# Performance work log

Measured on AMD Instinct MI355X. Metric: run time of the kernel, lower is better.

The kernel has to match this reference:

```python
import jax, jax.numpy as jnp
import numpy as np

D_MODEL = 1024
N_HEADS = 16
HEAD_DIM = D_MODEL // N_HEADS


def setup_inputs() -> dict:
    key = jax.random.key(0)
    kx, kq, kk, kv, ko = jax.random.split(key, 5)
    B, T = 4, 2048
    s = 1.0 / np.sqrt(D_MODEL)
    return {
        "x": jax.random.normal(kx, (B, T, D_MODEL), dtype=jnp.float32),
        "W_Q": jax.random.normal(kq, (D_MODEL, D_MODEL), dtype=jnp.float32) * s,
        "W_K": jax.random.normal(kk, (D_MODEL, D_MODEL), dtype=jnp.float32) * s,
        "W_V": jax.random.normal(kv, (D_MODEL, D_MODEL), dtype=jnp.float32) * s,
        "W_O": jax.random.normal(ko, (D_MODEL, D_MODEL), dtype=jnp.float32) * s,
    }


def reference(x, W_Q, W_K, W_V, W_O):
    B, T, C = x.shape
    H, hd = N_HEADS, HEAD_DIM
    # nn.Linear applies x @ W.T; W_* here are the [out,in] weight matrices.
    def proj(W):
        return (x @ W.T).reshape(B, T, H, hd).transpose(0, 2, 1, 3)  # [B,H,T,hd]
    q, k, v = proj(W_Q), proj(W_K), proj(W_V)
    scale = 1.0 / np.sqrt(hd).astype(np.float32)
    attn = jnp.einsum("bhqd,bhkd->bhqk", q, k) * scale  # [B,H,T,T]
    causal = jnp.tril(jnp.ones((T, T), dtype=bool))
    attn = jnp.where(causal, attn, -jnp.inf)
    attn = jax.nn.softmax(attn, axis=-1)
    out = jnp.einsum("bhqk,bhkd->bhqd", attn, v)  # [B,H,T,hd]
    out = out.transpose(0, 2, 1, 3).reshape(B, T, C)
    return out @ W_O.T
```

## Files before the change

kernel.cpp:

```cpp
#include <hip/hip_runtime.h>
#include <hip/hip_bf16.h>
#include <stdint.h>


typedef __attribute__((ext_vector_type(8))) short short8;
typedef __attribute__((ext_vector_type(4))) short short4v;
typedef __attribute__((ext_vector_type(4))) float floatx4;

#define LOG2E 1.4426950408889634f

__device__ __forceinline__ void gload_lds16(const void* g, void* l) {
  __builtin_amdgcn_global_load_lds(
      (const __attribute__((address_space(1))) void*)g,
      (__attribute__((address_space(3))) void*)l, 16, 0, 0);
}

__device__ __forceinline__ short f2bf(float f) {
  __hip_bfloat16 h = __float2bfloat16(f);
  return *reinterpret_cast<short*>(&h);
}

__global__ __launch_bounds__(256) void cvt_f32_bf16(const float* __restrict__ src,
                                                    short* __restrict__ dst, int n4,
                                                    float scale) {
  const int i = blockIdx.x * blockDim.x + threadIdx.x;
  if (i >= n4) return;
  const float4 v = reinterpret_cast<const float4*>(src)[i];
  short4v o;
  o.x = f2bf(v.x * scale); o.y = f2bf(v.y * scale);
  o.z = f2bf(v.z * scale); o.w = f2bf(v.w * scale);
  reinterpret_cast<short4v*>(dst)[i] = o;
}

__global__ __launch_bounds__(256) void cvt_weights(const float* __restrict__ wq,
                                                   const float* __restrict__ wk,
                                                   const float* __restrict__ wv,
                                                   const float* __restrict__ wo,
                                                   short* __restrict__ dst0,
                                                   float qscale) {
  const int y = blockIdx.y;
  const float* src = (y == 0) ? wq : (y == 1) ? wk : (y == 2) ? wv : wo;
  const float scale = (y == 0) ? qscale : 1.0f;
  short* dst = dst0 + (size_t)y * 1048576;
  const int i = blockIdx.x * blockDim.x + threadIdx.x;
  const float4 v = reinterpret_cast<const float4*>(src)[i];
  short4v o;
  o.x = f2bf(v.x * scale); o.y = f2bf(v.y * scale);
  o.z = f2bf(v.z * scale); o.w = f2bf(v.w * scale);
  reinterpret_cast<short4v*>(&dst[i * 4])[0] = o;
}

template <int MODE>
__device__ __forceinline__ void gemm256_body(const short* __restrict__ A,
                                             const short* __restrict__ B,
                                             void* __restrict__ Cout,
                                             int m0, int n0,
                                             short* __restrict__ la0,
                                             short* __restrict__ la1,
                                             short* __restrict__ la2,
                                             short* __restrict__ lb0,
                                             short* __restrict__ lb1,
                                             short* __restrict__ lb2) {
  const int tid = threadIdx.x;
  const int lane = tid & 63;
  const int w = tid >> 6;
  const int wm = w >> 1, wn = w & 1;
  const int lrow = lane & 15, lgrp = lane >> 4;

  floatx4 acc[4][4] = {};

  const int srow = tid >> 3;
  const int scb = (tid & 7) ^ (srow & 7);
  const short* ag = A + (size_t)(m0 + srow) * 1024 + scb * 8;
  const short* bg = B + (size_t)(n0 + srow) * 1024 + scb * 8;

  auto stage6 = [&](short* la, short* lb) {
    gload_lds16(ag, la + tid * 8);
    gload_lds16(ag + 64 * 1024, la + (512 + tid) * 8);
    gload_lds16(ag + 128 * 1024, la + (1024 + tid) * 8);
    gload_lds16(ag + 192 * 1024, la + (1536 + tid) * 8);
    gload_lds16(bg, lb + tid * 8);
    gload_lds16(bg + 64 * 1024, lb + (512 + tid) * 8);
    ag += 64; bg += 64;
  };

  short8 af[2][4];
  auto loadA = [&](const short* la) {
#pragma unroll
    for (int mf = 0; mf < 4; ++mf) {
      const int row = wm * 64 + mf * 16 + lrow;
#pragma unroll
      for (int kk = 0; kk < 2; ++kk)
        af[kk][mf] = *reinterpret_cast<const short8*>(
            &la[row * 64 + (((kk * 4 + lgrp) ^ (row & 7)) * 8)]);
    }
  };
  auto half = [&](const short* lb, int nh) {
    short8 bf[2][2];
#pragma unroll
    for (int nf = 0; nf < 2; ++nf) {
      const int row = wn * 64 + (nh * 2 + nf) * 16 + lrow;
#pragma unroll
      for (int kk = 0; kk < 2; ++kk)
        bf[kk][nf] = *reinterpret_cast<const short8*>(
            &lb[row * 64 + (((kk * 4 + lgrp) ^ (row & 7)) * 8)]);
    }
    __builtin_amdgcn_s_setprio(1);
#pragma unroll
    for (int kk = 0; kk < 2; ++kk)
#pragma unroll
      for (int mf = 0; mf < 4; ++mf)
#pragma unroll
        for (int nf = 0; nf < 2; ++nf)
          acc[mf][nh * 2 + nf] = __builtin_amdgcn_mfma_f32_16x16x32_bf16(
              af[kk][mf], bf[kk][nf], acc[mf][nh * 2 + nf], 0, 0, 0);
    __builtin_amdgcn_s_setprio(0);
  };
  auto compute = [&](const short* la, const short* lb) {
    loadA(la);
    half(lb, 0);
    half(lb, 1);
  };
  auto iter_main = [&](const short* ca, const short* cb, short* na, short* nb) {
    __builtin_amdgcn_sched_barrier(0);
    asm volatile("s_waitcnt vmcnt(6)" ::: "memory");
    __builtin_amdgcn_s_barrier();
    __builtin_amdgcn_sched_barrier(0);
    stage6(na, nb);
    compute(ca, cb);
  };

  stage6(la0, lb0);
  stage6(la1, lb1);

#pragma unroll 1
  for (int kt = 0; kt < 12; kt += 3) {
    iter_main(la0, lb0, la2, lb2);
    iter_main(la1, lb1, la0, lb0);
    iter_main(la2, lb2, la1, lb1);
  }
  iter_main(la0, lb0, la2, lb2);
  iter_main(la1, lb1, la0, lb0);
  {
    __builtin_amdgcn_sched_barrier(0);
    asm volatile("s_waitcnt vmcnt(6)" ::: "memory");
    __builtin_amdgcn_s_barrier();
    __builtin_amdgcn_sched_barrier(0);
    compute(la2, lb2);
  }
  {
    __builtin_amdgcn_sched_barrier(0);
    asm volatile("s_waitcnt vmcnt(0)" ::: "memory");
    __builtin_amdgcn_s_barrier();
    __builtin_amdgcn_sched_barrier(0);
    compute(la0, lb0);
  }

#pragma unroll
  for (int mf = 0; mf < 4; ++mf) {
#pragma unroll
    for (int nf = 0; nf < 4; ++nf) {
      if (MODE == 2) {
        short4v pk;
#pragma unroll
        for (int r = 0; r < 4; ++r) pk[r] = f2bf(acc[mf][nf][r]);
        const int t0 = m0 + wm * 64 + mf * 16 + lgrp * 4;
        const int ch = n0 + wn * 64 + nf * 16 + lrow;
        const int bh = ((t0 >> 11) << 4) + (ch >> 6);
        short* Vt = reinterpret_cast<short*>(Cout);
        *reinterpret_cast<short4v*>(
            &Vt[(size_t)bh * 131072 + (size_t)(ch & 63) * 2048 + (t0 & 2047)]) = pk;
      } else {
#pragma unroll
        for (int r = 0; r < 4; ++r) {
          const int grow = m0 + wm * 64 + mf * 16 + lgrp * 4 + r;
          const int gcol = n0 + wn * 64 + nf * 16 + lrow;
          if (MODE == 1)
            reinterpret_cast<short*>(Cout)[(size_t)grow * 1024 + gcol] = f2bf(acc[mf][nf][r]);
          else
            reinterpret_cast<float*>(Cout)[(size_t)grow * 1024 + gcol] = acc[mf][nf][r];
        }
      }
    }
  }
}

__global__ __launch_bounds__(512) void gemm_qkv(
    const short* __restrict__ xb, const short* __restrict__ wq, const short* __restrict__ wk,
    const short* __restrict__ wv, short* __restrict__ Qb, short* __restrict__ Kb,
    short* __restrict__ Vt) {
  __shared__ short lds_a[3][256 * 64];
  __shared__ short lds_b[3][128 * 64];
  const int flat = blockIdx.x;
  const int xcd = flat & 7, rest = flat >> 3;
  const int nblk = rest & 7, pg = rest >> 3;
  const int panel = pg * 8 + xcd;
  const int m = panel & 31, z = panel >> 5;
  const int m0 = m * 256, n0 = nblk * 128;
  if (z == 0)
    gemm256_body<1>(xb, wq, Qb, m0, n0, lds_a[0], lds_a[1], lds_a[2],
                    lds_b[0], lds_b[1], lds_b[2]);
  else if (z == 1)
    gemm256_body<1>(xb, wk, Kb, m0, n0, lds_a[0], lds_a[1], lds_a[2],
                    lds_b[0], lds_b[1], lds_b[2]);
  else
    gemm256_body<2>(xb, wv, Vt, m0, n0, lds_a[0], lds_a[1], lds_a[2],
                    lds_b[0], lds_b[1], lds_b[2]);
}

__global__ __launch_bounds__(512) void gemm_out(const short* __restrict__ Ob,
                                                const short* __restrict__ wo,
                                                float* __restrict__ out) {
  __shared__ short lds_a[3][256 * 64];
  __shared__ short lds_b[3][128 * 64];
  const int flat = blockIdx.x;
  const int xcd = flat & 7, rest = flat >> 3;
  const int nblk = rest & 7, pg = rest >> 3;
  const int panel = pg * 8 + xcd;
  gemm256_body<0>(Ob, wo, out, panel * 256, nblk * 128,
                  lds_a[0], lds_a[1], lds_a[2], lds_b[0], lds_b[1], lds_b[2]);
}

__global__ __launch_bounds__(256, 4) void attn_fwd(const short* __restrict__ Q,
                                                   const short* __restrict__ K,
                                                   const short* __restrict__ Vt,
                                                   short* __restrict__ O) {
  __shared__ short lds_k[2][64 * 64];
  __shared__ short lds_v[2][64 * 64];
  __shared__ short lds_p[4][16 * 64];

  const int tid = threadIdx.x;
  const int lane = tid & 63;
  const int w = tid >> 6;
  const int lrow = lane & 15, lgrp = lane >> 4;
  const int flat = blockIdx.x;
  const int bh = flat & 63;
  const int p = flat >> 6;
  const int b = bh >> 4, h = bh & 15;

  const size_t base = (size_t)b * 2048 * 1024 + h * 64;
  const size_t vbase = (size_t)bh * 131072;

  const int srow = tid >> 3;
  const int scb = (tid & 7) ^ (srow & 7);
  const size_t koff = (size_t)srow * 1024 + scb * 8;
  const size_t voff = (size_t)srow * 2048 + scb * 8;
  short* const kd0 = &lds_k[0][tid * 8];
  short* const kd1 = &lds_k[1][tid * 8];
  short* const vd0 = &lds_v[0][tid * 8];
  short* const vd1 = &lds_v[1][tid * 8];

  auto stageK = [&](short* ldst, const short* gsrc) {
    gload_lds16(gsrc, ldst);
    gload_lds16(gsrc + 32 * 1024, ldst + 2048);
  };
  auto stageV = [&](short* ldst, const short* gsrc) {
    gload_lds16(gsrc, ldst);
    gload_lds16(gsrc + 32 * 2048, ldst + 2048);
  };

#pragma unroll 1
  for (int pass = 0; pass < 2; ++pass) {
    const int qc = pass == 0 ? (31 - p) : p;
    const int qw = qc * 64 + w * 16;
    const int nkb = qc + 1;

    short8 qf0, qf1;
    {
      const short* qp = Q + base + (size_t)(qw + lrow) * 1024 + lgrp * 8;
      qf0 = *reinterpret_cast<const short8*>(qp);
      qf1 = *reinterpret_cast<const short8*>(qp + 32);
    }

    floatx4 oacc[4] = {};
    float lsum = 0.f;

    const short* kg = K + base + koff;
    const short* vg = Vt + vbase + voff;

    auto body = [&](int kb, const short* __restrict__ ldsk,
                    const short* __restrict__ ldsv) {
      floatx4 s[4];
      __builtin_amdgcn_s_setprio(1);
#pragma unroll
      for (int nf = 0; nf < 4; ++nf) {
        const short8 kf0 = *reinterpret_cast<const short8*>(
            &ldsk[(nf * 16 + lrow) * 64 + ((lgrp) ^ (lrow & 7)) * 8]);
        const short8 kf1 = *reinterpret_cast<const short8*>(
            &ldsk[(nf * 16 + lrow) * 64 + ((4 + lgrp) ^ (lrow & 7)) * 8]);
        floatx4 z = {};
        z = __builtin_amdgcn_mfma_f32_16x16x32_bf16(kf0, qf0, z, 0, 0, 0);
        z = __builtin_amdgcn_mfma_f32_16x16x32_bf16(kf1, qf1, z, 0, 0, 0);
        s[nf] = z;
      }
      __builtin_amdgcn_s_setprio(0);

      if (kb == qc) {
#pragma unroll
        for (int nf = 0; nf < 4; ++nf)
#pragma unroll
          for (int r = 0; r < 4; ++r)
            if (nf * 16 + lgrp * 4 + r > w * 16 + lrow) s[nf][r] = -1e30f;
      }

#pragma unroll
      for (int nf = 0; nf < 4; ++nf) {
        const float p0 = __builtin_amdgcn_exp2f(s[nf][0]);
        const float p1 = __builtin_amdgcn_exp2f(s[nf][1]);
        const float p2 = __builtin_amdgcn_exp2f(s[nf][2]);
        const float p3 = __builtin_amdgcn_exp2f(s[nf][3]);
        lsum += (p0 + p1) + (p2 + p3);
        short4v pk;
        pk.x = f2bf(p0); pk.y = f2bf(p1); pk.z = f2bf(p2); pk.w = f2bf(p3);
        const int c8 = (nf * 4 + lgrp) ^ ((lrow & 7) << 1);
        *reinterpret_cast<short4v*>(&lds_p[w][lrow * 64 + c8 * 4]) = pk;
      }

      short8 pa0, pa1;
      {
        const int c0 = (lgrp) ^ (lrow & 7);
        const int c1 = (4 + lgrp) ^ (lrow & 7);
        pa0 = *reinterpret_cast<const short8*>(&lds_p[w][lrow * 64 + c0 * 8]);
        pa1 = *reinterpret_cast<const short8*>(&lds_p[w][lrow * 64 + c1 * 8]);
      }
      __builtin_amdgcn_s_setprio(1);
#pragma unroll
      for (int nf = 0; nf < 4; ++nf) {
        const short8 vf0 = *reinterpret_cast<const short8*>(
            &ldsv[(nf * 16 + lrow) * 64 + ((lgrp) ^ (lrow & 7)) * 8]);
        const short8 vf1 = *reinterpret_cast<const short8*>(
            &ldsv[(nf * 16 + lrow) * 64 + ((4 + lgrp) ^ (lrow & 7)) * 8]);
        oacc[nf] = __builtin_amdgcn_mfma_f32_16x16x32_bf16(pa0, vf0, oacc[nf], 0, 0, 0);
        oacc[nf] = __builtin_amdgcn_mfma_f32_16x16x32_bf16(pa1, vf1, oacc[nf], 0, 0, 0);
      }
      __builtin_amdgcn_s_setprio(0);
    };

    stageK(kd0, kg); kg += 65536;
    stageV(vd0, vg); vg += 64;
    __syncthreads();

#pragma unroll 1
    for (int kb = 0; kb < nkb; kb += 2) {
      if (kb + 1 < nkb) { stageK(kd1, kg); kg += 65536; stageV(vd1, vg); vg += 64; }
      body(kb, lds_k[0], lds_v[0]);
      __syncthreads();
      if (kb + 1 >= nkb) break;
      if (kb + 2 < nkb) { stageK(kd0, kg); kg += 65536; stageV(vd0, vg); vg += 64; }
      body(kb + 1, lds_k[1], lds_v[1]);
      __syncthreads();
    }

    lsum += __shfl_xor(lsum, 16, 64);
    lsum += __shfl_xor(lsum, 32, 64);
#pragma unroll
    for (int r = 0; r < 4; ++r) {
      const float linv = 1.0f / __shfl(lsum, lgrp * 4 + r, 64);
      const int t = qw + lgrp * 4 + r;
#pragma unroll
      for (int nf = 0; nf < 4; ++nf)
        O[base + (size_t)t * 1024 + nf * 16 + lrow] = f2bf(oacc[nf][r] * linv);
    }
  }
}

extern "C" void kernel_launch(void* const* d_in, const int* in_sizes, int n_in,
                              void* d_out, int out_size, void* d_ws, size_t ws_size,
                              hipStream_t stream) {
  const float* x  = (const float*)d_in[0];
  const float* Wq = (const float*)d_in[1];
  const float* Wk = (const float*)d_in[2];
  const float* Wv = (const float*)d_in[3];
  const float* Wo = (const float*)d_in[4];

  uint8_t* ws = (uint8_t*)d_ws;
  short* xb  = (short*)(ws + 0);
  short* wqb = (short*)(ws + 16777216);
  short* wkb = (short*)(ws + 18874368);
  short* wvb = (short*)(ws + 20971520);
  short* wob = (short*)(ws + 23068672);
  short* Qb  = (short*)(ws + 25165824);
  short* Kb  = (short*)(ws + 41943040);
  short* Vt  = (short*)(ws + 58720256);
  short* Ob  = (short*)(ws + 75497472);
  if (ws_size < 92274688ull) return;

  const float qscale = 0.125f * LOG2E;

  cvt_f32_bf16<<<8192, 256, 0, stream>>>(x, xb, 2097152, 1.0f);
  cvt_weights<<<dim3(1024, 4), 256, 0, stream>>>(Wq, Wk, Wv, Wo, wqb, qscale);

  gemm_qkv<<<768, 512, 0, stream>>>(xb, wqb, wkb, wvb, Qb, Kb, Vt);
  attn_fwd<<<1024, 256, 0, stream>>>(Qb, Kb, Vt, Ob);
  gemm_out<<<256, 512, 0, stream>>>(Ob, wob, (float*)d_out);
}
```

Baseline: 159.2 us.

## Interleave LDS reads, prefetch issues and MFMA quadrants with wave barriers in GEMM

Restructures the GEMM main loop. Each K-tile is now split into four MFMA quadrants, with LDS fragment reads and the global-to-LDS prefetch loads interleaved between them. Extra s_barrier calls keep the waves in lockstep, in a ping-pong style schedule. The aim is to overlap LDS traffic and global load issue with matrix-core work and to reduce register pressure by holding fewer fragments live. The cost is more barriers per tile, which can stall waves. The swizzle expression was also changed from row&7 to lrow&7.

```diff
diff --git a/kernel.cpp b/kernel.cpp
--- a/kernel.cpp
+++ b/kernel.cpp
@@ -84,50 +84,103 @@
     ag += 64; bg += 64;
   };
 
-  short8 af[2][4];
-  auto loadA = [&](const short* la) {
-#pragma unroll
-    for (int mf = 0; mf < 4; ++mf) {
-      const int row = wm * 64 + mf * 16 + lrow;
-#pragma unroll
-      for (int kk = 0; kk < 2; ++kk)
-        af[kk][mf] = *reinterpret_cast<const short8*>(
-            &la[row * 64 + (((kk * 4 + lgrp) ^ (row & 7)) * 8)]);
-    }
-  };
-  auto half = [&](const short* lb, int nh) {
-    short8 bf[2][2];
-#pragma unroll
-    for (int nf = 0; nf < 2; ++nf) {
-      const int row = wn * 64 + (nh * 2 + nf) * 16 + lrow;
-#pragma unroll
-      for (int kk = 0; kk < 2; ++kk)
-        bf[kk][nf] = *reinterpret_cast<const short8*>(
-            &lb[row * 64 + (((kk * 4 + lgrp) ^ (row & 7)) * 8)]);
-    }
+  auto rdA = [&](const short* la, int mf, int kk) {
+    const int row = wm * 64 + mf * 16 + lrow;
+    return *reinterpret_cast<const short8*>(
+        &la[row * 64 + (((kk * 4 + lgrp) ^ (lrow & 7)) * 8)]);
+  };
+  auto rdB = [&](const short* lb, int nf, int kk) {
+    const int row = wn * 64 + nf * 16 + lrow;
+    return *reinterpret_cast<const short8*>(
+        &lb[row * 64 + (((kk * 4 + lgrp) ^ (lrow & 7)) * 8)]);
+  };
+
+  auto tile = [&](const short* la, const short* lb, short* na, short* nb, bool pf) {
+    short8 a0[2][2], a1[2][2], b0[2][2], b1[2][2];
+#pragma unroll
+    for (int kk = 0; kk < 2; ++kk) {
+      a0[kk][0] = rdA(la, 0, kk); a0[kk][1] = rdA(la, 1, kk);
+      b0[kk][0] = rdB(lb, 0, kk); b0[kk][1] = rdB(lb, 1, kk);
+    }
+    if (pf) {
+      gload_lds16(ag, na + tid * 8);
+      gload_lds16(ag + 64 * 1024, na + (512 + tid) * 8);
+    }
+    __builtin_amdgcn_sched_barrier(0);
+    __builtin_amdgcn_s_barrier();
     __builtin_amdgcn_s_setprio(1);
 #pragma unroll
     for (int kk = 0; kk < 2; ++kk)
 #pragma unroll
-      for (int mf = 0; mf < 4; ++mf)
-#pragma unroll
-        for (int nf = 0; nf < 2; ++nf)
-          acc[mf][nh * 2 + nf] = __builtin_amdgcn_mfma_f32_16x16x32_bf16(
-              af[kk][mf], bf[kk][nf], acc[mf][nh * 2 + nf], 0, 0, 0);
+      for (int i = 0; i < 2; ++i)
+#pragma unroll
+        for (int j = 0; j < 2; ++j)
+          acc[i][j] = __builtin_amdgcn_mfma_f32_16x16x32_bf16(a0[kk][i], b0[kk][j], acc[i][j], 0, 0, 0);
     __builtin_amdgcn_s_setprio(0);
-  };
-  auto compute = [&](const short* la, const short* lb) {
-    loadA(la);
-    half(lb, 0);
-    half(lb, 1);
-  };
-  auto iter_main = [&](const short* ca, const short* cb, short* na, short* nb) {
-    __builtin_amdgcn_sched_barrier(0);
-    asm volatile("s_waitcnt vmcnt(6)" ::: "memory");
-    __builtin_amdgcn_s_barrier();
-    __builtin_amdgcn_sched_barrier(0);
-    stage6(na, nb);
-    compute(ca, cb);
+    __builtin_amdgcn_sched_barrier(0);
+    __builtin_amdgcn_s_barrier();
+#pragma unroll
+    for (int kk = 0; kk < 2; ++kk) {
+      b1[kk][0] = rdB(lb, 2, kk); b1[kk][1] = rdB(lb, 3, kk);
+    }
+    if (pf) {
+      gload_lds16(ag + 128 * 1024, na + (1024 + tid) * 8);
+      gload_lds16(ag + 192 * 1024, na + (1536 + tid) * 8);
+    }
+    __builtin_amdgcn_sched_barrier(0);
+    __builtin_amdgcn_s_barrier();
+    __builtin_amdgcn_s_setprio(1);
+#pragma unroll
+    for (int kk = 0; kk < 2; ++kk)
+#pragma unroll
+      for (int i = 0; i < 2; ++i)
+#pragma unroll
+        for (int j = 0; j < 2; ++j)
+          acc[i][2 + j] = __builtin_amdgcn_mfma_f32_16x16x32_bf16(a0[kk][i], b1[kk][j], acc[i][2 + j], 0, 0, 0);
+    __builtin_amdgcn_s_setprio(0);
+    __builtin_amdgcn_sched_barrier(0);
+    __builtin_amdgcn_s_barrier();
+#pragma unroll
+    for (int kk = 0; kk < 2; ++kk) {
+      a1[kk][0] = rdA(la, 2, kk); a1[kk][1] = rdA(la, 3, kk);
+    }
+    if (pf) {
+      gload_lds16(bg, nb + tid * 8);
+      gload_lds16(bg + 64 * 1024, nb + (512 + tid) * 8);
+      ag += 64; bg += 64;
+    }
+    __builtin_amdgcn_sched_barrier(0);
+    __builtin_amdgcn_s_barrier();
+    __builtin_amdgcn_s_setprio(1);
+#pragma unroll
+    for (int kk = 0; kk < 2; ++kk)
+#pragma unroll
+      for (int i = 0; i < 2; ++i)
+#pragma unroll
+        for (int j = 0; j < 2; ++j)
+          acc[2 + i][j] = __builtin_amdgcn_mfma_f32_16x16x32_bf16(a1[kk][i], b0[kk][j], acc[2 + i][j], 0, 0, 0);
+    __builtin_amdgcn_s_setprio(0);
+    __builtin_amdgcn_sched_barrier(0);
+    __builtin_amdgcn_s_barrier();
+    __builtin_amdgcn_s_setprio(1);
+#pragma unroll
+    for (int kk = 0; kk < 2; ++kk)
+#pragma unroll
+      for (int i = 0; i < 2; ++i)
+#pragma unroll
+        for (int j = 0; j < 2; ++j)
+          acc[2 + i][2 + j] = __builtin_amdgcn_mfma_f32_16x16x32_bf16(a1[kk][i], b1[kk][j], acc[2 + i][2 + j], 0, 0, 0);
+    __builtin_amdgcn_s_setprio(0);
+  };
+
+  auto tiletop = [&](int n) {
+    __builtin_amdgcn_sched_barrier(0);
+    if (n == 0)
+      asm volatile("s_waitcnt vmcnt(0)" ::: "memory");
+    else
+      asm volatile("s_waitcnt vmcnt(6)" ::: "memory");
+    __builtin_amdgcn_s_barrier();
+    __builtin_amdgcn_sched_barrier(0);
   };
 
   stage6(la0, lb0);
@@ -135,26 +188,14 @@
 
 #pragma unroll 1
   for (int kt = 0; kt < 12; kt += 3) {
-    iter_main(la0, lb0, la2, lb2);
-    iter_main(la1, lb1, la0, lb0);
-    iter_main(la2, lb2, la1, lb1);
+    tiletop(6); tile(la0, lb0, la2, lb2, true);
+    tiletop(6); tile(la1, lb1, la0, lb0, true);
+    tiletop(6); tile(la2, lb2, la1, lb1, true);
   }
-  iter_main(la0, lb0, la2, lb2);
-  iter_main(la1, lb1, la0, lb0);
-  {
-    __builtin_amdgcn_sched_barrier(0);
-    asm volatile("s_waitcnt vmcnt(6)" ::: "memory");
-    __builtin_amdgcn_s_barrier();
-    __builtin_amdgcn_sched_barrier(0);
-    compute(la2, lb2);
-  }
-  {
-    __builtin_amdgcn_sched_barrier(0);
-    asm volatile("s_waitcnt vmcnt(0)" ::: "memory");
-    __builtin_amdgcn_s_barrier();
-    __builtin_amdgcn_sched_barrier(0);
-    compute(la0, lb0);
-  }
+  tiletop(6); tile(la0, lb0, la2, lb2, true);
+  tiletop(6); tile(la1, lb1, la0, lb0, true);
+  tiletop(6); tile(la2, lb2, nullptr, nullptr, false);
+  tiletop(0); tile(la0, lb0, nullptr, nullptr, false);
 
 #pragma unroll
   for (int mf = 0; mf < 4; ++mf) {
```

Result: slower. 163.8 us (+2.9%).

## Halve GEMM K-tile to 32 with new LDS swizzle and deeper iteration count

Applied to the files above, without the earlier changes.

The shared GEMM body now stages K-tiles of 32 instead of 64 bf16 elements, which halves the LDS footprint per buffer and uses a 4-column XOR swizzle. Each tile issues 3 async global-to-LDS loads instead of 6 and runs 16 MFMAs per barrier, over 32 iterations instead of 16. The smaller LDS footprint could allow more blocks per CU. In exchange it doubles the number of barriers and waitcnt synchronisations per K sweep and shortens the prefetch distance in bytes.

```diff
diff --git a/kernel.cpp b/kernel.cpp
--- a/kernel.cpp
+++ b/kernel.cpp
@@ -69,92 +69,63 @@
 
   floatx4 acc[4][4] = {};
 
-  const int srow = tid >> 3;
-  const int scb = (tid & 7) ^ (srow & 7);
+  const int srow = tid >> 2;
+  const int scb = (tid & 3) ^ (srow & 3) ^ ((srow & 4) >> 1);
   const short* ag = A + (size_t)(m0 + srow) * 1024 + scb * 8;
   const short* bg = B + (size_t)(n0 + srow) * 1024 + scb * 8;
 
-  auto stage6 = [&](short* la, short* lb) {
+  auto stage3 = [&](short* la, short* lb) {
     gload_lds16(ag, la + tid * 8);
-    gload_lds16(ag + 64 * 1024, la + (512 + tid) * 8);
-    gload_lds16(ag + 128 * 1024, la + (1024 + tid) * 8);
-    gload_lds16(ag + 192 * 1024, la + (1536 + tid) * 8);
+    gload_lds16(ag + 128 * 1024, la + (512 + tid) * 8);
     gload_lds16(bg, lb + tid * 8);
-    gload_lds16(bg + 64 * 1024, lb + (512 + tid) * 8);
-    ag += 64; bg += 64;
-  };
-
-  short8 af[2][4];
-  auto loadA = [&](const short* la) {
+    ag += 32; bg += 32;
+  };
+
+  const int slA = (lgrp ^ (lrow & 3) ^ ((lrow & 4) >> 1)) * 8;
+
+  auto tile = [&](const short* la, const short* lb, short* na, short* nb, bool pf) {
+    if (pf) stage3(na, nb);
+    short8 af[4], bf[4];
 #pragma unroll
     for (int mf = 0; mf < 4; ++mf) {
       const int row = wm * 64 + mf * 16 + lrow;
-#pragma unroll
-      for (int kk = 0; kk < 2; ++kk)
-        af[kk][mf] = *reinterpret_cast<const short8*>(
-            &la[row * 64 + (((kk * 4 + lgrp) ^ (row & 7)) * 8)]);
-    }
-  };
-  auto half = [&](const short* lb, int nh) {
-    short8 bf[2][2];
-#pragma unroll
-    for (int nf = 0; nf < 2; ++nf) {
-      const int row = wn * 64 + (nh * 2 + nf) * 16 + lrow;
-#pragma unroll
-      for (int kk = 0; kk < 2; ++kk)
-        bf[kk][nf] = *reinterpret_cast<const short8*>(
-            &lb[row * 64 + (((kk * 4 + lgrp) ^ (row & 7)) * 8)]);
+      af[mf] = *reinterpret_cast<const short8*>(&la[row * 32 + slA]);
+    }
+#pragma unroll
+    for (int nf = 0; nf < 4; ++nf) {
+      const int row = wn * 64 + nf * 16 + lrow;
+      bf[nf] = *reinterpret_cast<const short8*>(&lb[row * 32 + slA]);
     }
     __builtin_amdgcn_s_setprio(1);
 #pragma unroll
-    for (int kk = 0; kk < 2; ++kk)
-#pragma unroll
-      for (int mf = 0; mf < 4; ++mf)
-#pragma unroll
-        for (int nf = 0; nf < 2; ++nf)
-          acc[mf][nh * 2 + nf] = __builtin_amdgcn_mfma_f32_16x16x32_bf16(
-              af[kk][mf], bf[kk][nf], acc[mf][nh * 2 + nf], 0, 0, 0);
+    for (int mf = 0; mf < 4; ++mf)
+#pragma unroll
+      for (int nf = 0; nf < 4; ++nf)
+        acc[mf][nf] = __builtin_amdgcn_mfma_f32_16x16x32_bf16(af[mf], bf[nf], acc[mf][nf], 0, 0, 0);
     __builtin_amdgcn_s_setprio(0);
   };
-  auto compute = [&](const short* la, const short* lb) {
-    loadA(la);
-    half(lb, 0);
-    half(lb, 1);
-  };
-  auto iter_main = [&](const short* ca, const short* cb, short* na, short* nb) {
+
+  auto tiletop = [&](int n) {
     __builtin_amdgcn_sched_barrier(0);
-    asm volatile("s_waitcnt vmcnt(6)" ::: "memory");
+    if (n == 0)
+      asm volatile("s_waitcnt vmcnt(0)" ::: "memory");
+    else
+      asm volatile("s_waitcnt vmcnt(3)" ::: "memory");
     __builtin_amdgcn_s_barrier();
     __builtin_amdgcn_sched_barrier(0);
-    stage6(na, nb);
-    compute(ca, cb);
-  };
-
-  stage6(la0, lb0);
-  stage6(la1, lb1);
+  };
+
+  stage3(la0, lb0);
+  stage3(la1, lb1);
 
 #pragma unroll 1
-  for (int kt = 0; kt < 12; kt += 3) {
-    iter_main(la0, lb0, la2, lb2);
-    iter_main(la1, lb1, la0, lb0);
-    iter_main(la2, lb2, la1, lb1);
+  for (int kt = 0; kt < 30; kt += 3) {
+    tiletop(3); tile(la0, lb0, la2, lb2, true);
+    tiletop(3); tile(la1, lb1, la0, lb0, true);
+    tiletop(3); tile(la2, lb2, la1, lb1, true);
   }
-  iter_main(la0, lb0, la2, lb2);
-  iter_main(la1, lb1, la0, lb0);
-  {
-    __builtin_amdgcn_sched_barrier(0);
-    asm volatile("s_waitcnt vmcnt(6)" ::: "memory");
-    __builtin_amdgcn_s_barrier();
-    __builtin_amdgcn_sched_barrier(0);
-    compute(la2, lb2);
-  }
-  {
-    __builtin_amdgcn_sched_barrier(0);
-    asm volatile("s_waitcnt vmcnt(0)" ::: "memory");
-    __builtin_amdgcn_s_barrier();
-    __builtin_amdgcn_sched_barrier(0);
-    compute(la0, lb0);
-  }
+  tiletop(3); tile(la0, lb0, nullptr, nullptr, false);
+  tiletop(0); tile(la1, lb1, nullptr, nullptr, false);
 
 #pragma unroll
   for (int mf = 0; mf < 4; ++mf) {
@@ -189,8 +160,8 @@
     const short* __restrict__ xb, const short* __restrict__ wq, const short* __restrict__ wk,
     const short* __restrict__ wv, short* __restrict__ Qb, short* __restrict__ Kb,
     short* __restrict__ Vt) {
-  __shared__ short lds_a[3][256 * 64];
-  __shared__ short lds_b[3][128 * 64];
+  __shared__ short lds_a[3][256 * 32];
+  __shared__ short lds_b[3][128 * 32];
   const int flat = blockIdx.x;
   const int xcd = flat & 7, rest = flat >> 3;
   const int nblk = rest & 7, pg = rest >> 3;
@@ -211,8 +182,8 @@
 __global__ __launch_bounds__(512) void gemm_out(const short* __restrict__ Ob,
                                                 const short* __restrict__ wo,
                                                 float* __restrict__ out) {
-  __shared__ short lds_a[3][256 * 64];
-  __shared__ short lds_b[3][128 * 64];
+  __shared__ short lds_a[3][256 * 32];
+  __shared__ short lds_b[3][128 * 32];
   const int flat = blockIdx.x;
   const int xcd = flat & 7, rest = flat >> 3;
   const int nblk = rest & 7, pg = rest >> 3;
```

Result: no change. 158.5 us (-0.4%).
